# Optimization experiments

Measured on AMD Instinct MI355X. Metric: run time of the kernel, lower is better.

Reference implementation:

```python
import jax, jax.numpy as jnp
from jax import lax
import numpy as np

B, C, H, W = 4, 256, 64, 64
O, KH, KW = 256, 3, 3
STR, PAD, DIL = 1, 1, 1
K = KH * KW
EPS = 1e-5


def setup_inputs() -> dict:
    key = jax.random.key(0)
    ks = jax.random.split(key, 8)
    fan = 1.0 / np.sqrt(C * KH * KW)
    return {
        "input_x": jax.random.normal(ks[0], (B, C, H, W), jnp.float32),
        # offset-generating conv (DeformConv2dPack style): 2*K channels of (dy, dx)
        "w_offset": jax.random.normal(ks[1], (2 * K, C, KH, KW), jnp.float32) * 0.01,
        "b_offset": jnp.zeros((2 * K,), jnp.float32),
        # deformable conv weight / bias
        "weight": jax.random.normal(ks[2], (O, C, KH, KW), jnp.float32) * fan,
        "bias": jax.random.normal(ks[3], (O,), jnp.float32) * 0.01,
        # BatchNorm2d params + running stats (inference mode)
        "gamma": jax.random.normal(ks[4], (O,), jnp.float32) * 0.1 + 1.0,
        "beta": jax.random.normal(ks[5], (O,), jnp.float32) * 0.1,
        "run_mean": jax.random.normal(ks[6], (O,), jnp.float32) * 0.1,
        "run_var": jax.random.uniform(ks[7], (O,), jnp.float32, 0.5, 1.5),
    }


def _bilinear_sample(img, y, x):
    """img: [B,C,H,W]; y,x: [B,K,Ho,Wo] float sample coords. Zero outside."""
    y0 = jnp.floor(y)
    x0 = jnp.floor(x)
    ly = y - y0
    lx = x - x0
    y0i = y0.astype(jnp.int32)
    x0i = x0.astype(jnp.int32)
    y1i = y0i + 1
    x1i = x0i + 1

    def valid(yi, xi):
        return ((yi >= 0) & (yi < H) & (xi >= 0) & (xi < W)).astype(img.dtype)

    # per-corner interpolation weights, zeroed when the corner is out of bounds
    w00 = (1 - ly) * (1 - lx) * valid(y0i, x0i)
    w01 = (1 - ly) * lx * valid(y0i, x1i)
    w10 = ly * (1 - lx) * valid(y1i, x0i)
    w11 = ly * lx * valid(y1i, x1i)

    y0c = jnp.clip(y0i, 0, H - 1)
    y1c = jnp.clip(y1i, 0, H - 1)
    x0c = jnp.clip(x0i, 0, W - 1)
    x1c = jnp.clip(x1i, 0, W - 1)

    gather = jax.vmap(lambda im, yi, xi: im[:, yi, xi])  # -> [B,C,K,Ho,Wo]
    out = gather(img, y0c, x0c) * w00[:, None]
    out = out + gather(img, y0c, x1c) * w01[:, None]
    out = out + gather(img, y1c, x0c) * w10[:, None]
    out = out + gather(img, y1c, x1c) * w11[:, None]
    return out  # [B,C,K,Ho,Wo]


def reference(input_x, w_offset, b_offset, weight, bias, gamma, beta, run_mean, run_var):
    # 1) generate offsets with a regular conv (DeformConv2dPack conv_offset)
    offset = lax.conv_general_dilated(
        input_x, w_offset, (STR, STR), [(PAD, PAD), (PAD, PAD)],
        rhs_dilation=(DIL, DIL), dimension_numbers=("NCHW", "OIHW", "NCHW"))
    offset = offset + b_offset[None, :, None, None]  # [B, 2K, Ho, Wo]
    Ho, Wo = offset.shape[2], offset.shape[3]
    off = offset.reshape(B, K, 2, Ho, Wo)
    dy, dx = off[:, :, 0], off[:, :, 1]  # [B,K,Ho,Wo]

    # 2) base sampling grid for each kernel tap
    ky, kx = jnp.meshgrid(jnp.arange(KH), jnp.arange(KW), indexing="ij")
    base_y = (jnp.arange(Ho) * STR - PAD)[None, :, None] + (ky.reshape(-1) * DIL)[:, None, None]
    base_x = (jnp.arange(Wo) * STR - PAD)[None, None, :] + (kx.reshape(-1) * DIL)[:, None, None]
    y = base_y.astype(input_x.dtype) + dy  # [B,K,Ho,Wo]
    x = base_x.astype(input_x.dtype) + dx

    # 3) bilinear-sampled im2col then dense contraction
    sampled = _bilinear_sample(input_x, y, x)  # [B,C,K,Ho,Wo]
    out = jnp.einsum("bckhw,ock->bohw", sampled, weight.reshape(O, C, K))
    out = out + bias[None, :, None, None]

    # 4) BatchNorm (inference, running stats) + ReLU
    inv = gamma / jnp.sqrt(run_var + EPS)
    out = out * inv[None, :, None, None] + (beta - run_mean * inv)[None, :, None, None]
    return jax.nn.relu(out)
```

## Files before the change

### kernel.cpp

```cpp
#include <hip/hip_runtime.h>
#include <math.h>

typedef __attribute__((ext_vector_type(8))) short b8;
typedef __attribute__((ext_vector_type(4))) float f4;
typedef float f4u __attribute__((ext_vector_type(4), aligned(4)));
typedef _Float16 h8 __attribute__((ext_vector_type(8)));
typedef _Float16 h2 __attribute__((ext_vector_type(2)));

#define XT2   0
#define OF2   2097152
#define WH2   2392064
#define WL2   2428928
#define AF2   3571712
#define BF2   3866624

__device__ inline ushort f2bf(float f) {
  uint u = __float_as_uint(f);
  return (ushort)((u + 0x7FFFu + ((u >> 16) & 1u)) >> 16);
}
__device__ inline h2 u2h2(uint u) { union { uint u; h2 h; } x; x.u = u; return x.h; }
__device__ inline uint h22u(h2 h) { union { uint u; h2 h; } x; x.h = h; return x.u; }
__device__ inline uint duph(float f) {
  union { _Float16 h; ushort u; } x; x.h = (_Float16)f;
  return ((uint)x.u << 16) | x.u;
}

__global__ __launch_bounds__(256) void pre_k(
    const float* __restrict__ x, const float* __restrict__ w,
    const float* __restrict__ wof, const float* __restrict__ bias,
    const float* __restrict__ gamma, const float* __restrict__ beta,
    const float* __restrict__ mean, const float* __restrict__ var,
    float* __restrict__ ws) {
  const int bid = blockIdx.x;
  if (bid < 2048) {
    const int id  = bid * 256 + threadIdx.x;
    const int p   = id & 4095;
    const int cg8 = (id >> 12) & 31;
    const int b   = id >> 17;
    const float* xp = x + (((long)(b * 256 + cg8 * 8)) << 12) + p;
    _Float16* xt = (_Float16*)(ws + XT2);
    h8 pk;
#pragma unroll
    for (int j = 0; j < 8; ++j) pk[j] = (_Float16)xp[(long)j << 12];
    *(h8*)(xt + ((((long)(b << 12) + p)) << 8) + (cg8 << 3)) = pk;
    return;
  }
  const int tid = (bid - 2048) * 256 + threadIdx.x;
  const int l  = tid & 63;
  const int ot = (tid >> 6) & 15;
  const int f  = tid >> 10;
  const int o  = (ot << 4) + (l & 15);
  const float inv = gamma[o] * rsqrtf(var[o] + 1e-5f);
  {
    const int s  = f & 1;
    const int g  = f >> 1;
    const int cw = g / 9;
    const int kk = g - cw * 9;
    const int cb = (cw << 6) + (s << 5) + ((l >> 4) << 3);
    h8 pk;
#pragma unroll
    for (int j = 0; j < 8; ++j)
      pk[j] = (_Float16)(w[((o << 8) + cb + j) * 9 + kk] * inv);
    *(h8*)((_Float16*)(ws + AF2) + tid * 8) = pk;
    ((f4*)(ws + OF2))[tid] = f4{0.f, 0.f, 0.f, 0.f};
  }
  if (tid < 256) {
    const float iv = gamma[tid] * rsqrtf(var[tid] + 1e-5f);
    ws[BF2 + tid] = bias[tid] * iv + beta[tid] - mean[tid] * iv;
  }
  if (tid < 9216) {
    const int l2  = tid & 63;
    const int mt  = (tid >> 6) & 1;
    const int i2  = tid >> 7;
    const int cg2 = i2 / 9;
    const int kk2 = i2 - cg2 * 9;
    const int oc  = (mt << 4) + (l2 & 15);
    const int cb2 = (cg2 << 5) + ((l2 >> 4) << 3);
    b8 ph, pl;
#pragma unroll
    for (int j = 0; j < 8; ++j) {
      const float v = (oc < 18) ? wof[((oc << 8) + cb2 + j) * 9 + kk2] : 0.f;
      const ushort h = f2bf(v);
      const float hf = __uint_as_float((uint)h << 16);
      ph[j] = (short)h;
      pl[j] = (short)f2bf(v - hf);
    }
    *(b8*)((short*)(ws + WH2) + tid * 8) = ph;
    *(b8*)((short*)(ws + WL2) + tid * 8) = pl;
  }
}

__global__ __launch_bounds__(256, 4) void offset_part_k(
    const float* __restrict__ x, float* __restrict__ ws) {
  __shared__ __align__(16) ushort Xh[3][66][40];
  __shared__ __align__(16) ushort Xl[3][66][40];
  const int bid = blockIdx.x;
  const int q   = bid >> 8;
  const int b   = (bid >> 6) & 3;
  const int ho  = bid & 63;
  const int t   = threadIdx.x;
  const int l   = t & 63;
  const int wv  = t >> 6;
  const short* afh = (const short*)(ws + WH2);
  const short* afl = (const short*)(ws + WL2);

  for (int u = t; u < 240; u += 256) {
    const int row = u / 80, rem = u % 80;
    const int col = (rem >= 40) ? 65 : 0;
    const int c   = rem % 40;
    Xh[row][col][c] = 0;
    Xl[row][col][c] = 0;
  }

  f4 acc[2];
  acc[0] = f4{0.f, 0.f, 0.f, 0.f};
  acc[1] = f4{0.f, 0.f, 0.f, 0.f};

  const int cidx = t >> 3;
  const int j8   = t & 7;
  const float* xc = x + ((long)b << 20) + ((long)cidx << 12);
  const int col = (wv << 4) + (l & 15);
  const int qc  = (l >> 4) << 3;

  for (int it = 0; it < 2; ++it) {
    const int cg = (q << 1) + it;
    __syncthreads();
    const float* xg = xc + ((long)(cg << 5) << 12);
#pragma unroll
    for (int rep = 0; rep < 6; ++rep) {
      const int fi   = (rep << 3) + j8;
      const int row  = fi >> 4;
      const int colf = (fi & 15) << 2;
      const int y = ho - 1 + row;
      f4u v = {0.f, 0.f, 0.f, 0.f};
      if (y >= 0 && y <= 63) v = *(const f4u*)(xg + (y << 6) + colf);
#pragma unroll
      for (int qq = 0; qq < 4; ++qq) {
        const ushort h = f2bf(v[qq]);
        const float hf = __uint_as_float((uint)h << 16);
        Xh[row][colf + 1 + qq][cidx] = h;
        Xl[row][colf + 1 + qq][cidx] = f2bf(v[qq] - hf);
      }
    }
    __syncthreads();
#pragma unroll
    for (int kk = 0; kk < 9; ++kk) {
      const int ky = kk / 3, kx = kk - ky * 3;
      const int i  = cg * 9 + kk;
      const b8 ah0 = *(const b8*)(afh + ((((i << 1) + 0) << 6) + l) * 8);
      const b8 ah1 = *(const b8*)(afh + ((((i << 1) + 1) << 6) + l) * 8);
      const b8 al0 = *(const b8*)(afl + ((((i << 1) + 0) << 6) + l) * 8);
      const b8 al1 = *(const b8*)(afl + ((((i << 1) + 1) << 6) + l) * 8);
      const b8 bh = *(const b8*)&Xh[ky][col + kx][qc];
      const b8 bl = *(const b8*)&Xl[ky][col + kx][qc];
      acc[0] = __builtin_amdgcn_mfma_f32_16x16x32_bf16(ah0, bh, acc[0], 0, 0, 0);
      acc[0] = __builtin_amdgcn_mfma_f32_16x16x32_bf16(ah0, bl, acc[0], 0, 0, 0);
      acc[0] = __builtin_amdgcn_mfma_f32_16x16x32_bf16(al0, bh, acc[0], 0, 0, 0);
      acc[1] = __builtin_amdgcn_mfma_f32_16x16x32_bf16(ah1, bh, acc[1], 0, 0, 0);
      acc[1] = __builtin_amdgcn_mfma_f32_16x16x32_bf16(ah1, bl, acc[1], 0, 0, 0);
      acc[1] = __builtin_amdgcn_mfma_f32_16x16x32_bf16(al1, bh, acc[1], 0, 0, 0);
    }
  }

  const int wo = col;
  const int q4 = (l >> 4) << 2;
#pragma unroll
  for (int mt = 0; mt < 2; ++mt)
#pragma unroll
    for (int r = 0; r < 4; ++r) {
      const int oc = (mt << 4) + q4 + r;
      if (oc < 18)
        atomicAdd(&ws[OF2 + ((b * 18 + oc) << 12) + (ho << 6) + wo],
                  acc[mt][r]);
    }
}

__global__ __launch_bounds__(256, 2) void deform_gemm_f16b(
    const float* __restrict__ ws, const float* __restrict__ bof,
    float* __restrict__ out) {
  __shared__ __align__(16) uint Bs[3][32][32];
  __shared__ uint4 dW[288];
  __shared__ int4  dP[288];

  const int t     = threadIdx.x;
  const int bid   = blockIdx.x;
  const int xcd   = bid & 7;
  const int batch = xcd >> 1;
  const int half  = xcd & 1;
  const int j     = bid >> 3;
  const int sp0   = (half << 11) + (j << 5);
  const int l     = t & 63;
  const int wv    = t >> 6;

  const int sn  = ((wv & 1) << 4) | (l & 15);
  const int cg8 = ((wv >> 1) << 2) | (l >> 4);
  const uint* xtu = (const uint*)(ws + XT2) + ((long)batch << 19);
  const _Float16* af = (const _Float16*)(ws + AF2);

  for (int u = t; u < 288; u += 256) {
    const int kk = u >> 5, s = u & 31;
    const int sp = sp0 + s;
    const int ho = sp >> 6, wo = sp & 63;
    const int ky = kk / 3, kx = kk - ky * 3;
    const float dy =
        ws[OF2 + ((batch * 18 + (kk << 1)) << 12) + sp] + bof[kk << 1];
    const float dx =
        ws[OF2 + ((batch * 18 + (kk << 1) + 1) << 12) + sp] + bof[(kk << 1) + 1];
    const float py = (float)(ho - 1 + ky) + dy;
    const float px = (float)(wo - 1 + kx) + dx;
    const float y0f = floorf(py), x0f = floorf(px);
    const float ly = py - y0f, lx = px - x0f;
    const int y0 = (int)y0f, x0 = (int)x0f;
    const int y1 = y0 + 1, x1 = x0 + 1;
    const float vy0 = (y0 >= 0 && y0 < 64) ? 1.f : 0.f;
    const float vy1 = (y1 >= 0 && y1 < 64) ? 1.f : 0.f;
    const float vx0 = (x0 >= 0 && x0 < 64) ? 1.f : 0.f;
    const float vx1 = (x1 >= 0 && x1 < 64) ? 1.f : 0.f;
    const int y0c = min(max(y0, 0), 63), y1c = min(max(y1, 0), 63);
    const int x0c = min(max(x0, 0), 63), x1c = min(max(x1, 0), 63);
    uint4 wv4;
    wv4.x = duph((1.f - ly) * (1.f - lx) * vy0 * vx0);
    wv4.y = duph((1.f - ly) * lx * vy0 * vx1);
    wv4.z = duph(ly * (1.f - lx) * vy1 * vx0);
    wv4.w = duph(ly * lx * vy1 * vx1);
    int4 pv;
    pv.x = (y0c << 6) + x0c;
    pv.y = (y0c << 6) + x1c;
    pv.z = (y1c << 6) + x0c;
    pv.w = (y1c << 6) + x1c;
    dW[u] = wv4;
    dP[u] = pv;
  }
  __syncthreads();

  f4 acc[4][2];
#pragma unroll
  for (int m = 0; m < 4; ++m)
#pragma unroll
    for (int nt = 0; nt < 2; ++nt) acc[m][nt] = f4{0.f, 0.f, 0.f, 0.f};

  uint4 cset0[4], cset1[4];
  uint4 w0v, w1v, wq; int4 pq;
  h8 aA[4][2], aN[4][2];
  int kkd, kkg, cwg, bufc;

#define FRDD(W_, P_, KK_) do { const int u_ = ((KK_) << 5) + sn;             \
    W_ = dW[u_]; P_ = dP[u_]; } while (0)

#define FGATH(DST_, P_) do {                                                 \
    const int co_ = (cwg << 5) + (cg8 << 2);                                 \
    DST_[0] = *(const uint4*)(xtu + ((P_).x << 7) + co_);                    \
    DST_[1] = *(const uint4*)(xtu + ((P_).y << 7) + co_);                    \
    DST_[2] = *(const uint4*)(xtu + ((P_).z << 7) + co_);                    \
    DST_[3] = *(const uint4*)(xtu + ((P_).w << 7) + co_);                    \
  } while (0)

#define FCOMB(CS_, WV_, BUF_) do {                                           \
    const h2 wc0_ = u2h2((WV_).x), wc1_ = u2h2((WV_).y);                     \
    const h2 wc2_ = u2h2((WV_).z), wc3_ = u2h2((WV_).w);                     \
    uint4 r_;                                                                \
    r_.x = h22u(u2h2(CS_[0].x) * wc0_ + u2h2(CS_[1].x) * wc1_ +              \
                u2h2(CS_[2].x) * wc2_ + u2h2(CS_[3].x) * wc3_);              \
    r_.y = h22u(u2h2(CS_[0].y) * wc0_ + u2h2(CS_[1].y) * wc1_ +              \
                u2h2(CS_[2].y) * wc2_ + u2h2(CS_[3].y) * wc3_);              \
    r_.z = h22u(u2h2(CS_[0].z) * wc0_ + u2h2(CS_[1].z) * wc1_ +              \
                u2h2(CS_[2].z) * wc2_ + u2h2(CS_[3].z) * wc3_);              \
    r_.w = h22u(u2h2(CS_[0].w) * wc0_ + u2h2(CS_[1].w) * wc1_ +              \
                u2h2(CS_[2].w) * wc2_ + u2h2(CS_[3].w) * wc3_);              \
    *(uint4*)&Bs[BUF_][sn][(cg8 ^ (sn & 7)) << 2] = r_;                      \
  } while (0)

#define FLOADA(I_, DST_) do {                                                \
    _Pragma("unroll")                                                        \
    for (int m = 0; m < 4; ++m)                                              \
      _Pragma("unroll")                                                      \
      for (int s = 0; s < 2; ++s) {                                          \
        const int f_ = ((I_) << 1) + s;                                      \
        DST_[m][s] = *(const h8*)(af +                                       \
            ((((f_ << 4) + (wv << 2) + m) << 6) + l) * 8);                   \
      }                                                                      \
  } while (0)

#define FMFMA(AC_, BUF_) do {                                                \
    h8 bB_[2][2];                                                            \
    _Pragma("unroll")                                                        \
    for (int nt = 0; nt < 2; ++nt)                                           \
      _Pragma("unroll")                                                      \
      for (int s = 0; s < 2; ++s) {                                          \
        const int snr_ = (nt << 4) + (l & 15);                               \
        const int ph_  = (((s << 2) + (l >> 4)) ^ (snr_ & 7)) << 2;          \
        bB_[nt][s] = *(const h8*)&Bs[BUF_][snr_][ph_];                       \
      }                                                                      \
    _Pragma("unroll")                                                        \
    for (int m = 0; m < 4; ++m)                                              \
      _Pragma("unroll")                                                      \
      for (int nt = 0; nt < 2; ++nt) {                                       \
        acc[m][nt] = __builtin_amdgcn_mfma_f32_16x16x32_f16(                 \
            AC_[m][0], bB_[nt][0], acc[m][nt], 0, 0, 0);                     \
        acc[m][nt] = __builtin_amdgcn_mfma_f32_16x16x32_f16(                 \
            AC_[m][1], bB_[nt][1], acc[m][nt], 0, 0, 0);                     \
      }                                                                      \
  } while (0)

#define FBODY(I_, AC_, AN_, CC_, WC_, CN_, WN_) do {                         \
    if ((I_) < 34) {                                                         \
      WN_ = wq; FGATH(CN_, pq);                                              \
      kkg++; if (kkg == 9) { kkg = 0; cwg++; }                               \
    }                                                                        \
    if ((I_) < 33) { FRDD(wq, pq, kkd); kkd = (kkd == 8) ? 0 : kkd + 1; }    \
    const int bufn_ = (bufc == 2) ? 0 : bufc + 1;                            \
    FMFMA(AC_, bufc);                                                        \
    if ((I_) < 35) {                                                         \
      FLOADA((I_) + 1, AN_);                                                 \
      FCOMB(CC_, WC_, bufn_);                                                \
    }                                                                        \
    bufc = bufn_;                                                            \
    __syncthreads();                                                         \
  } while (0)

  {
    uint4 wA; int4 pA;
    cwg = 0;
    FRDD(wA, pA, 0);
    FGATH(cset0, pA);
    FRDD(w1v, pA, 1);
    FGATH(cset1, pA);
    FRDD(wq, pq, 2);
    FLOADA(0, aA);
    FCOMB(cset0, wA, 0);
    kkd = 3; kkg = 2; bufc = 0;
  }
  __syncthreads();

  for (int i = 0; i < 36; i += 2) {
    FBODY(i,     aA, aN, cset1, w1v, cset0, w0v);
    FBODY(i + 1, aN, aA, cset0, w0v, cset1, w1v);
  }

  const float* bfold = ws + BF2;
  const int quad = l >> 4;
  const int ow = wv << 6;
#pragma unroll
  for (int m = 0; m < 4; ++m) {
    const int ob = ow + (m << 4) + (quad << 2);
    const f4 bf = *(const f4*)&bfold[ob];
#pragma unroll
    for (int nt = 0; nt < 2; ++nt) {
      const int sp = sp0 + (nt << 4) + (l & 15);
#pragma unroll
      for (int r = 0; r < 4; ++r) {
        out[(((batch << 8) + ob + r) << 12) + sp] =
            fmaxf(acc[m][nt][r] + bf[r], 0.f);
      }
    }
  }
}

extern "C" void kernel_launch(void* const* d_in, const int* in_sizes, int n_in,
                              void* d_out, int out_size, void* d_ws, size_t ws_size,
                              hipStream_t stream) {
  const float* x     = (const float*)d_in[0];
  const float* wof   = (const float*)d_in[1];
  const float* bof   = (const float*)d_in[2];
  const float* w     = (const float*)d_in[3];
  const float* bias  = (const float*)d_in[4];
  const float* gamma = (const float*)d_in[5];
  const float* beta  = (const float*)d_in[6];
  const float* mean  = (const float*)d_in[7];
  const float* var   = (const float*)d_in[8];
  float* out = (float*)d_out;
  float* ws  = (float*)d_ws;

  hipLaunchKernelGGL(pre_k, dim3(2336), dim3(256), 0, stream,
                     x, w, wof, bias, gamma, beta, mean, var, ws);
  hipLaunchKernelGGL(offset_part_k, dim3(1024), dim3(256), 0, stream, x, ws);
  hipLaunchKernelGGL(deform_gemm_f16b, dim3(512), dim3(256), 0, stream,
                     ws, bof, out);
}
```

Baseline: 156.5 us.

## Overlap input transpose and weight packing with offset conv in one launch

Moves the fp16 transposed copy of x and the BN-folded weight packing out of the prep kernel and into the offset-conv kernel as extra blocks, interleaved two transpose blocks per offset-conv block. The prep kernel shrinks to zeroing the offset buffer and packing the offset weights. The aim is to overlap memory-bound conversion work with the MFMA offset conv and cut one serialized phase. The mixed kernel keeps the large shared-memory footprint for every block, which may limit occupancy for the light conversion blocks.

```diff
diff --git a/kernel.cpp b/kernel.cpp
--- a/kernel.cpp
+++ b/kernel.cpp
@@ -25,45 +25,13 @@
   return ((uint)x.u << 16) | x.u;
 }
 
-__global__ __launch_bounds__(256) void pre_k(
-    const float* __restrict__ x, const float* __restrict__ w,
+__global__ __launch_bounds__(256) void prep0_k(
     const float* __restrict__ wof, const float* __restrict__ bias,
     const float* __restrict__ gamma, const float* __restrict__ beta,
     const float* __restrict__ mean, const float* __restrict__ var,
     float* __restrict__ ws) {
-  const int bid = blockIdx.x;
-  if (bid < 2048) {
-    const int id  = bid * 256 + threadIdx.x;
-    const int p   = id & 4095;
-    const int cg8 = (id >> 12) & 31;
-    const int b   = id >> 17;
-    const float* xp = x + (((long)(b * 256 + cg8 * 8)) << 12) + p;
-    _Float16* xt = (_Float16*)(ws + XT2);
-    h8 pk;
-#pragma unroll
-    for (int j = 0; j < 8; ++j) pk[j] = (_Float16)xp[(long)j << 12];
-    *(h8*)(xt + ((((long)(b << 12) + p)) << 8) + (cg8 << 3)) = pk;
-    return;
-  }
-  const int tid = (bid - 2048) * 256 + threadIdx.x;
-  const int l  = tid & 63;
-  const int ot = (tid >> 6) & 15;
-  const int f  = tid >> 10;
-  const int o  = (ot << 4) + (l & 15);
-  const float inv = gamma[o] * rsqrtf(var[o] + 1e-5f);
-  {
-    const int s  = f & 1;
-    const int g  = f >> 1;
-    const int cw = g / 9;
-    const int kk = g - cw * 9;
-    const int cb = (cw << 6) + (s << 5) + ((l >> 4) << 3);
-    h8 pk;
-#pragma unroll
-    for (int j = 0; j < 8; ++j)
-      pk[j] = (_Float16)(w[((o << 8) + cb + j) * 9 + kk] * inv);
-    *(h8*)((_Float16*)(ws + AF2) + tid * 8) = pk;
-    ((f4*)(ws + OF2))[tid] = f4{0.f, 0.f, 0.f, 0.f};
-  }
+  const int tid = blockIdx.x * 256 + threadIdx.x;
+  ((f4*)(ws + OF2))[tid] = f4{0.f, 0.f, 0.f, 0.f};
   if (tid < 256) {
     const float iv = gamma[tid] * rsqrtf(var[tid] + 1e-5f);
     ws[BF2 + tid] = bias[tid] * iv + beta[tid] - mean[tid] * iv;
@@ -90,15 +58,54 @@
   }
 }
 
-__global__ __launch_bounds__(256, 4) void offset_part_k(
-    const float* __restrict__ x, float* __restrict__ ws) {
+__global__ __launch_bounds__(256, 4) void mid_k(
+    const float* __restrict__ x, const float* __restrict__ w,
+    const float* __restrict__ gamma, const float* __restrict__ var,
+    float* __restrict__ ws) {
   __shared__ __align__(16) ushort Xh[3][66][40];
   __shared__ __align__(16) ushort Xl[3][66][40];
   const int bid = blockIdx.x;
-  const int q   = bid >> 8;
-  const int b   = (bid >> 6) & 3;
-  const int ho  = bid & 63;
   const int t   = threadIdx.x;
+
+  if (bid >= 3072) {
+    const int tid = (bid - 3072) * 256 + t;
+    const int l  = tid & 63;
+    const int ot = (tid >> 6) & 15;
+    const int f  = tid >> 10;
+    const int o  = (ot << 4) + (l & 15);
+    const float inv = gamma[o] * rsqrtf(var[o] + 1e-5f);
+    const int s  = f & 1;
+    const int g  = f >> 1;
+    const int cw = g / 9;
+    const int kk = g - cw * 9;
+    const int cb = (cw << 6) + (s << 5) + ((l >> 4) << 3);
+    h8 pk;
+#pragma unroll
+    for (int j = 0; j < 8; ++j)
+      pk[j] = (_Float16)(w[((o << 8) + cb + j) * 9 + kk] * inv);
+    *(h8*)((_Float16*)(ws + AF2) + tid * 8) = pk;
+    return;
+  }
+
+  const int r = bid % 3;
+  const int g = bid / 3;
+  if (r != 2) {
+    const int id  = ((g << 1) + r) * 256 + t;
+    const int p   = id & 4095;
+    const int cg8 = (id >> 12) & 31;
+    const int b   = id >> 17;
+    const float* xp = x + (((long)(b * 256 + cg8 * 8)) << 12) + p;
+    _Float16* xt = (_Float16*)(ws + XT2);
+    h8 pk;
+#pragma unroll
+    for (int j = 0; j < 8; ++j) pk[j] = (_Float16)xp[(long)j << 12];
+    *(h8*)(xt + ((((long)(b << 12) + p)) << 8) + (cg8 << 3)) = pk;
+    return;
+  }
+
+  const int q   = g >> 8;
+  const int b   = (g >> 6) & 3;
+  const int ho  = g & 63;
   const int l   = t & 63;
   const int wv  = t >> 6;
   const short* afh = (const short*)(ws + WH2);
@@ -167,11 +174,11 @@
 #pragma unroll
   for (int mt = 0; mt < 2; ++mt)
 #pragma unroll
-    for (int r = 0; r < 4; ++r) {
-      const int oc = (mt << 4) + q4 + r;
+    for (int rr = 0; rr < 4; ++rr) {
+      const int oc = (mt << 4) + q4 + rr;
       if (oc < 18)
         atomicAdd(&ws[OF2 + ((b * 18 + oc) << 12) + (ho << 6) + wo],
-                  acc[mt][r]);
+                  acc[mt][rr]);
     }
 }
 
@@ -348,9 +355,9 @@
     for (int nt = 0; nt < 2; ++nt) {
       const int sp = sp0 + (nt << 4) + (l & 15);
 #pragma unroll
-      for (int r = 0; r < 4; ++r) {
-        out[(((batch << 8) + ob + r) << 12) + sp] =
-            fmaxf(acc[m][nt][r] + bf[r], 0.f);
+      for (int rr = 0; rr < 4; ++rr) {
+        out[(((batch << 8) + ob + rr) << 12) + sp] =
+            fmaxf(acc[m][nt][rr] + bf[rr], 0.f);
       }
     }
   }
@@ -371,9 +378,10 @@
   float* out = (float*)d_out;
   float* ws  = (float*)d_ws;
 
-  hipLaunchKernelGGL(pre_k, dim3(2336), dim3(256), 0, stream,
-                     x, w, wof, bias, gamma, beta, mean, var, ws);
-  hipLaunchKernelGGL(offset_part_k, dim3(1024), dim3(256), 0, stream, x, ws);
+  hipLaunchKernelGGL(prep0_k, dim3(288), dim3(256), 0, stream,
+                     wof, bias, gamma, beta, mean, var, ws);
+  hipLaunchKernelGGL(mid_k, dim3(3360), dim3(256), 0, stream,
+                     x, w, gamma, var, ws);
   hipLaunchKernelGGL(deform_gemm_f16b, dim3(512), dim3(256), 0, stream,
                      ws, bof, out);
 }
```

New measurement: 154.2 us. No clear change (-1.5%).
